# Kernel tuning notes

Measured on AMD Instinct MI355X. Metric: run time of the kernel, lower is better.

The kernel has to match this reference:

```python
import jax, jax.numpy as jnp
import numpy as np

TAU = 0.1
B = 4        # number of batches
S = 256      # spatial extent per axis
K = 128      # max peaks per batch (original caps total at num_batches*128)
NEG = -jnp.inf


def _l2norm(x, eps=1e-12):
    n = jnp.sqrt(jnp.sum(x * x, axis=1, keepdims=True))
    return x / jnp.maximum(n, eps)


def _peak_pool(coords, feats, conf, mask):
    # Submanifold 3x3x3 sparse max-pool on conf and avg-pool on feats,
    # restricted to voxels with conf > tau (the original builds the spconv
    # tensors only from masked voxels). Neighbor lookup via sorted key hash.
    N = coords.shape[0]
    bidx = coords[:, 0]
    x, y, z = coords[:, 1], coords[:, 2], coords[:, 3]
    key = ((bidx * S + x) * S + y) * S + z
    order = jnp.argsort(key)
    skey = key[order]
    hmax = jnp.full((N,), NEG, dtype=conf.dtype)
    fsum = jnp.zeros_like(feats)
    cnt = jnp.zeros((N,), dtype=feats.dtype)
    for dx in (-1, 0, 1):
        for dy in (-1, 0, 1):
            for dz in (-1, 0, 1):
                nx, ny, nz = x + dx, y + dy, z + dz
                valid = (nx >= 0) & (nx < S) & (ny >= 0) & (ny < S) & (nz >= 0) & (nz < S)
                nkey = ((bidx * S + nx) * S + ny) * S + nz
                pos = jnp.minimum(jnp.searchsorted(skey, nkey), N - 1)
                j = order[pos]
                hit = valid & (skey[pos] == nkey) & mask[j]
                hmax = jnp.maximum(hmax, jnp.where(hit, conf[j], NEG))
                fsum = fsum + jnp.where(hit[:, None], feats[j], 0.0)
                cnt = cnt + hit.astype(feats.dtype)
    favg = fsum / jnp.maximum(cnt, 1.0)[:, None]
    return hmax, favg


def setup_inputs() -> dict:
    key = jax.random.key(0)
    ks = jax.random.split(key, 6)
    N, L, D = 800000, 64, 32
    batch = jax.random.randint(ks[0], (N, 1), 0, B, dtype=jnp.int32)
    xyz = jax.random.randint(ks[1], (N, 3), 0, S, dtype=jnp.int32)
    coords = jnp.concatenate([batch, xyz], axis=1)
    voxel_feats = jax.random.normal(ks[2], (N, L), jnp.float32)
    centroid_scores = jax.random.uniform(ks[3], (N, 1), jnp.float32)
    W = jax.random.normal(ks[4], (L, D), jnp.float32) * 0.05
    b = jnp.zeros((D,), jnp.float32)
    background = jax.random.normal(ks[5], (D,), jnp.float32) * 0.02
    return {"coords": coords, "voxel_feats": voxel_feats,
            "centroid_scores": centroid_scores, "W": W, "b": b,
            "background": background}


def reference(coords, voxel_feats, centroid_scores, W, b, background):
    conf = centroid_scores[:, 0]
    mask = conf > TAU
    hmax, peak_feats = _peak_pool(coords, voxel_feats, conf, mask)
    # CenterNet-style NMS: a masked voxel is a peak if it equals its local max
    peak_mask = mask & (hmax == conf)
    voxel_desc = _l2norm(voxel_feats @ W + b)           # [N, D]
    bidx = coords[:, 0]
    peak_conf, blocks = [], []
    for bi in range(B):
        score = jnp.where(peak_mask & (bidx == bi), conf, NEG)
        vals, idx = jax.lax.top_k(score, K)             # fixed K peaks/batch
        valid = jnp.isfinite(vals)
        cdesc = _l2norm(peak_feats[idx] @ W + b)        # [K, D]
        cdesc = jnp.where(valid[:, None], cdesc, 0.0)
        # per-batch layout: background descriptor first, then centroids
        blocks.append(jnp.concatenate([background[None, :], cdesc], axis=0))
        peak_conf.append(jnp.where(valid, vals, 0.0))
    full_desc = jnp.concatenate(blocks, axis=0)         # [B*(K+1), D]
    return jnp.stack(peak_conf, axis=0), voxel_desc, full_desc
```

## Files before the change

kernel.cpp:

```cpp
#include <hip/hip_runtime.h>
#include <math.h>

#define S 256
#define NB 4
#define TAU 0.1f
#define KSEL 128
#define LOG_TAB 21
#define TAB_SZ (1u << LOG_TAB)
#define TAB_MASK (TAB_SZ - 1)
#define EMPTY64 0xFFFFFFFFFFFFFFFFull
#define BM_WORDS (1u << 21)
#define NBINS 8192
#define BIN_BASE 0x3D800
#define CAND_CAP 4096
#define CPAD 32

typedef unsigned long long u64;
typedef unsigned int u32;

__device__ __forceinline__ u32 hash_key(int key) {
    u32 h = (u32)key * 0x9E3779B1u;
    h ^= h >> 15;
    return h & TAB_MASK;
}

__device__ __forceinline__ int conf_bin(float conf) {
    int bin = (int)(__float_as_uint(conf) >> 12) - BIN_BASE;
    return bin < 0 ? 0 : (bin > NBINS - 1 ? NBINS - 1 : bin);
}

__device__ __forceinline__ int tab_lookup(const u64* __restrict__ tab, int key) {
    u32 slot = hash_key(key);
    for (;;) {
        u64 e = tab[slot];
        if ((u32)(e >> 32) == (u32)key) return (int)(u32)e;
        if (e == EMPTY64) return -1;
        slot = (slot + 1) & TAB_MASK;
    }
}

__device__ __forceinline__ void desc_row(const float* __restrict__ feats,
                                         const float* __restrict__ W,
                                         const float* __restrict__ bias,
                                         float* __restrict__ voxel_desc, int i, int N) {
    if (i >= N) return;
    const float4* row4 = (const float4*)(feats + (size_t)i * 64);
    float4 r[16];
    #pragma unroll
    for (int k = 0; k < 16; k++) r[k] = row4[k];
    __builtin_amdgcn_sched_barrier(0);
    float acc[32];
    #pragma unroll
    for (int d = 0; d < 32; d++) acc[d] = bias[d];
    #pragma unroll
    for (int k = 0; k < 16; k++) {
        float4 f = r[k];
        const float* Wb = W + k * 4 * 32;
        #pragma unroll
        for (int d = 0; d < 32; d++) {
            acc[d] = fmaf(f.x, Wb[d], acc[d]);
            acc[d] = fmaf(f.y, Wb[32 + d], acc[d]);
            acc[d] = fmaf(f.z, Wb[64 + d], acc[d]);
            acc[d] = fmaf(f.w, Wb[96 + d], acc[d]);
        }
    }
    float ss = 0.f;
    #pragma unroll
    for (int d = 0; d < 32; d++) ss += acc[d] * acc[d];
    float inv = 1.0f / fmaxf(sqrtf(ss), 1e-12f);
    float4* out4 = (float4*)(voxel_desc + (size_t)i * 32);
    #pragma unroll
    for (int q = 0; q < 8; q++) {
        float4 o;
        o.x = acc[q * 4 + 0] * inv; o.y = acc[q * 4 + 1] * inv;
        o.z = acc[q * 4 + 2] * inv; o.w = acc[q * 4 + 3] * inv;
        out4[q] = o;
    }
}

__device__ __forceinline__ void insert_pt(const int* __restrict__ coords,
                                          const float* __restrict__ scores,
                                          u64* __restrict__ tab, u32* __restrict__ bm,
                                          int i, int N) {
    if (i >= N) return;
    int4 c = ((const int4*)coords)[i];
    float conf = scores[i];
    int key = ((c.x * S + c.y) * S + c.z) * S + c.w;
    if (conf > TAU) atomicOr(&bm[(u32)key >> 5], 1u << (key & 31));
    u64 ins = ((u64)(u32)key << 32) | (u32)i;
    u32 slot = hash_key(key);
    for (;;) {
        u64 e = tab[slot];
        if ((u32)(e >> 32) == (u32)key) { atomicMin(&tab[slot], ins); return; }
        if (e == EMPTY64) {
            u64 prev = atomicCAS(&tab[slot], EMPTY64, ins);
            if (prev == EMPTY64) return;
            if ((u32)(prev >> 32) == (u32)key) { atomicMin(&tab[slot], ins); return; }
        }
        slot = (slot + 1) & TAB_MASK;
    }
}

__global__ __launch_bounds__(256, 4) void k_ins_desc(const int* __restrict__ coords,
        const float* __restrict__ scores, u64* __restrict__ tab, u32* __restrict__ bm,
        const float* __restrict__ feats, const float* __restrict__ W,
        const float* __restrict__ bias, float* __restrict__ voxel_desc,
        int N, int nIns, int nDesc, int descRow0) {
    int g = blockIdx.x / 3, r = blockIdx.x % 3;
    if (r < 2) {
        int ib = g * 2 + r;
        if (ib >= nIns) return;
        insert_pt(coords, scores, tab, bm, ib * 256 + threadIdx.x, N);
    } else {
        if (g >= nDesc) return;
        desc_row(feats, W, bias, voxel_desc, descRow0 + g * 256 + threadIdx.x, N);
    }
}

__device__ __forceinline__ void peak_block(const int* __restrict__ coords,
        const float* __restrict__ scores, const u64* __restrict__ tab,
        const u32* __restrict__ bm, u64* __restrict__ peaks, int* __restrict__ cnt,
        int* __restrict__ hist, int N, int pcap, int pb) {
    int i = pb * 256 + threadIdx.x;
    bool alive = (i < N);
    int ii = alive ? i : 0;
    int4 c = ((const int4*)coords)[ii];
    float conf = alive ? scores[ii] : -1.0f;
    int kb = ((c.x * S + c.y) * S + c.z) * S + c.w;
    bool ispeak = false;
    if (alive && conf > TAU) {
        u32 m27 = 0;
        u32 vzm = (u32)((c.w > 0) ? 1 : 0) | 2u | (u32)((c.w < S - 1) ? 4 : 0);
        #pragma unroll
        for (int dx = -1; dx <= 1; dx++) {
            if ((unsigned)(c.y + dx) >= S) continue;
            #pragma unroll
            for (int dy = -1; dy <= 1; dy++) {
                if ((unsigned)(c.z + dy) >= S) continue;
                int nk = kb + dx * (S * S) + dy * S;
                u32 idx = (u32)nk >> 5;
                int sft = nk & 31;
                u32 w0 = bm[idx];
                u32 b3;
                if (sft >= 1 && sft <= 30) {
                    b3 = (w0 >> (sft - 1)) & 7u;
                } else if (sft == 0) {
                    u32 wm = (nk >= 32) ? bm[idx - 1] : 0u;
                    b3 = ((wm >> 31) & 1u) | ((w0 & 3u) << 1);
                } else {
                    u32 wp = (idx + 1 < BM_WORDS) ? bm[idx + 1] : 0u;
                    b3 = ((w0 >> 30) & 3u) | ((wp & 1u) << 2);
                }
                b3 &= vzm;
                int p = ((dx + 1) * 3 + (dy + 1)) * 3;
                m27 |= b3 << p;
            }
        }
        int j0 = tab_lookup(tab, kb);
        float hmax = (j0 == i) ? conf : scores[j0];
        m27 &= ~(1u << 13);
        while (m27) {
            int q = __builtin_ctz(m27);
            m27 &= m27 - 1;
            int dx = q / 9 - 1;
            int rr = q % 9;
            int dy = rr / 3 - 1, dz = rr % 3 - 1;
            int j = tab_lookup(tab, kb + dx * (S * S) + dy * S + dz);
            if (j >= 0) hmax = fmaxf(hmax, scores[j]);
        }
        ispeak = (hmax == conf);
    }

    if (ispeak) atomicAdd(&hist[c.x * NBINS + conf_bin(conf)], 1);

    __shared__ int wcnt[4][NB];
    __shared__ int bbase[NB];
    int w = threadIdx.x >> 6;
    int lane = threadIdx.x & 63;
    u64 lmask_lt = (lane == 63) ? 0x7FFFFFFFFFFFFFFFull : ((1ull << lane) - 1ull);
    u64 mb[NB];
    #pragma unroll
    for (int b = 0; b < NB; b++) {
        mb[b] = __ballot(ispeak && (c.x == b));
        if (lane == 0) wcnt[w][b] = __popcll(mb[b]);
    }
    __syncthreads();
    if (threadIdx.x < NB) {
        int b = threadIdx.x;
        int tot = wcnt[0][b] + wcnt[1][b] + wcnt[2][b] + wcnt[3][b];
        bbase[b] = tot > 0 ? atomicAdd(&cnt[b * CPAD], tot) : 0;
    }
    __syncthreads();
    if (ispeak) {
        int b = c.x;
        int pre = 0;
        for (int w2 = 0; w2 < w; w2++) pre += wcnt[w2][b];
        int rank = __popcll(mb[b] & lmask_lt);
        int pidx = bbase[b] + pre + rank;
        if (pidx < pcap)
            peaks[(size_t)b * pcap + pidx] =
                ((u64)__float_as_uint(conf) << 32) | (u32)(~(u32)i);
    }
}

__global__ __launch_bounds__(256, 4) void k_peak_desc(const int* __restrict__ coords,
        const float* __restrict__ scores, const u64* __restrict__ tab,
        const u32* __restrict__ bm, u64* __restrict__ peaks, int* __restrict__ cnt,
        int* __restrict__ hist, const float* __restrict__ feats,
        const float* __restrict__ W, const float* __restrict__ bias,
        float* __restrict__ voxel_desc, int N, int pcap,
        int nPeak, int nDesc, int descRow0) {
    int g = blockIdx.x / 3, r = blockIdx.x % 3;
    if (r < 2) {
        int pb = g * 2 + r;
        if (pb >= nPeak) return;
        peak_block(coords, scores, tab, bm, peaks, cnt, hist, N, pcap, pb);
    } else {
        if (g >= nDesc) return;
        desc_row(feats, W, bias, voxel_desc, descRow0 + g * 256 + threadIdx.x, N);
    }
}

__global__ void k_thresh(const int* __restrict__ hist, const int* __restrict__ cnt,
                         u32* __restrict__ thrbin, int pcap) {
    int w = threadIdx.x >> 6;
    int lane = threadIdx.x & 63;
    if (w >= NB) return;
    int n = cnt[w * CPAD]; if (n > pcap) n = pcap;
    int need = n < KSEL ? n : KSEL;
    const int* h = hist + w * NBINS;
    int running = 0;
    u32 thr = 0;
    for (int hi = NBINS - 64; hi >= 0; hi -= 64) {
        int v = h[hi + lane];
        int s = v;
        #pragma unroll
        for (int off = 1; off < 64; off <<= 1) {
            int o = __shfl_down(s, off);
            if (lane + off < 64) s += o;
        }
        int csum = __shfl(s, 0);
        if (running + csum >= need) {
            u64 m = __ballot(running + s >= need);
            int top = 63 - __builtin_clzll(m);
            thr = (u32)(hi + top);
            break;
        }
        running += csum;
    }
    if (lane == 0) thrbin[w] = thr;
}

__global__ void k_compact(const u64* __restrict__ peaks, const int* __restrict__ cnt,
                          const u32* __restrict__ thrbin, u64* __restrict__ cand,
                          int* __restrict__ ccnt, int pcap) {
    int t = blockIdx.x * blockDim.x + threadIdx.x;
    int b = t / pcap;
    if (b >= NB) return;
    int e = t % pcap;
    int n = cnt[b * CPAD]; if (n > pcap) n = pcap;
    if (e >= n) return;
    u64 key = peaks[(size_t)b * pcap + e];
    float conf = __uint_as_float((u32)(key >> 32));
    if (conf_bin(conf) >= (int)thrbin[b]) {
        int p = atomicAdd(&ccnt[b * CPAD], 1);
        if (p < CAND_CAP) cand[(size_t)b * CAND_CAP + p] = key;
    }
}

__global__ void k_topk(u64* __restrict__ cand, const int* __restrict__ ccnt,
                       u64* __restrict__ bufA, u64* __restrict__ selected) {
    int b = blockIdx.x;
    int tid = threadIdx.x;
    __shared__ int hist[256];
    __shared__ int sh_split, sh_above, sh_selc, sh_candc;
    u64* sel = selected + b * KSEL;
    u64* pcur = cand + (size_t)b * CAND_CAP;
    u64* pnxt = bufA + (size_t)b * CAND_CAP;
    int n = ccnt[b * CPAD];
    if (n > CAND_CAP) n = CAND_CAP;
    int need = KSEL, nsel = 0;

    for (int byte = 7; byte >= 0; byte--) {
        if (need <= 0) break;
        if (n <= need) {
            for (int idx = tid; idx < n; idx += blockDim.x) sel[nsel + idx] = pcur[idx];
            nsel += n; need -= n; n = 0;
            break;
        }
        hist[tid] = 0;
        __syncthreads();
        int shift = byte * 8;
        for (int idx = tid; idx < n; idx += blockDim.x)
            atomicAdd(&hist[(int)((pcur[idx] >> shift) & 255)], 1);
        __syncthreads();
        if (tid == 0) {
            int above = 0, s = 255;
            for (; s > 0; s--) {
                if (above + hist[s] >= need) break;
                above += hist[s];
            }
            sh_split = s; sh_above = above; sh_selc = 0; sh_candc = 0;
        }
        __syncthreads();
        int s = sh_split;
        for (int idx = tid; idx < n; idx += blockDim.x) {
            u64 e = pcur[idx];
            int bv = (int)((e >> shift) & 255);
            if (bv > s) { int p = atomicAdd(&sh_selc, 1); sel[nsel + p] = e; }
            else if (bv == s) { int p = atomicAdd(&sh_candc, 1); pnxt[p] = e; }
        }
        __syncthreads();
        nsel += sh_above; need -= sh_above; n = sh_candc;
        u64* t = pcur; pcur = pnxt; pnxt = t;
        __syncthreads();
    }
    if (need > 0 && n > 0) {
        int take = need < n ? need : n;
        for (int idx = tid; idx < take; idx += blockDim.x) sel[nsel + idx] = pcur[idx];
        nsel += take;
    }
    for (int idx = nsel + tid; idx < KSEL; idx += blockDim.x) sel[idx] = 0;
    __syncthreads();

    __shared__ u64 sk[KSEL];
    if (tid < KSEL) sk[tid] = sel[tid];
    __syncthreads();
    for (int k = 2; k <= KSEL; k <<= 1) {
        for (int j = k >> 1; j > 0; j >>= 1) {
            if (tid < KSEL) {
                int ixj = tid ^ j;
                if (ixj > tid) {
                    u64 a = sk[tid], c2 = sk[ixj];
                    bool upper = (tid & k) != 0;
                    if (upper ? (a > c2) : (a < c2)) { sk[tid] = c2; sk[ixj] = a; }
                }
            }
            __syncthreads();
        }
    }
    if (tid < KSEL) sel[tid] = sk[tid];
}

__global__ void k_final(const int* __restrict__ coords, const float* __restrict__ feats,
                        const float* __restrict__ scores, const float* __restrict__ W,
                        const float* __restrict__ bias, const float* __restrict__ background,
                        const u64* __restrict__ tab, const u64* __restrict__ selected,
                        float* __restrict__ out, int N) {
    int gw = (blockIdx.x * blockDim.x + threadIdx.x) >> 6;
    int lane = threadIdx.x & 63;
    float* full = out + NB * KSEL + (size_t)N * 32;
    if (gw >= NB * KSEL) {
        int b = gw - NB * KSEL;
        if (b < NB && lane < 32)
            full[(size_t)(b * (KSEL + 1)) * 32 + lane] = background[lane];
        return;
    }
    int b = gw >> 7, k = gw & 127;
    u64 key = selected[gw];
    float* row = full + (size_t)(b * (KSEL + 1) + 1 + k) * 32;
    if (key == 0ull) {
        if (lane == 0) out[gw] = 0.f;
        if (lane < 32) row[lane] = 0.f;
        return;
    }
    float conf = __uint_as_float((u32)(key >> 32));
    int i = (int)(~(u32)key);
    if (lane == 0) out[gw] = conf;
    int4 c = ((const int4*)coords)[i];
    int kb = ((c.x * S + c.y) * S + c.z) * S + c.w;
    int j = -1; bool hit = false;
    if (lane < 27) {
        int dx = lane / 9 - 1, r = lane % 9;
        int dy = r / 3 - 1, dz = r % 3 - 1;
        int nx = c.y + dx, ny = c.z + dy, nz = c.w + dz;
        if ((unsigned)nx < S && (unsigned)ny < S && (unsigned)nz < S) {
            j = tab_lookup(tab, kb + dx * (S * S) + dy * S + dz);
            if (j >= 0) hit = scores[j] > TAU;
        }
    }
    u64 hm = __ballot(hit);
    int c27 = __popcll(hm);
    float fsum = 0.f;
    u64 m = hm;
    while (m) {
        int src = __ffsll((long long)m) - 1;
        m &= m - 1;
        int jj = __shfl(j, src);
        fsum += feats[(size_t)jj * 64 + lane];
    }
    float favg = fsum / fmaxf((float)c27, 1.0f);
    int d = lane & 31;
    float acc = bias[d];
    #pragma unroll
    for (int l = 0; l < 64; l++) {
        float fl = __shfl(favg, l);
        acc = fmaf(fl, W[l * 32 + d], acc);
    }
    float ss = acc * acc;
    #pragma unroll
    for (int off = 1; off < 32; off <<= 1) ss += __shfl_xor(ss, off);
    float inv = 1.0f / fmaxf(sqrtf(ss), 1e-12f);
    if (lane < 32) row[lane] = acc * inv;
}

extern "C" void kernel_launch(void* const* d_in, const int* in_sizes, int n_in,
                              void* d_out, int out_size, void* d_ws, size_t ws_size,
                              hipStream_t stream) {
    const int* coords = (const int*)d_in[0];
    const float* feats = (const float*)d_in[1];
    const float* scores = (const float*)d_in[2];
    const float* W = (const float*)d_in[3];
    const float* bias = (const float*)d_in[4];
    const float* background = (const float*)d_in[5];
    int N = in_sizes[0] / 4;
    float* out = (float*)d_out;
    int pcap = N / 2;

    char* ws = (char*)d_ws;
    size_t off = 0;
    u64* tab = (u64*)(ws + off); off += (size_t)TAB_SZ * 8;
    size_t zoff = off;
    u32* bm = (u32*)(ws + off); off += (size_t)BM_WORDS * 4;
    int* hist = (int*)(ws + off); off += (size_t)NB * NBINS * 4;
    int* cnt = (int*)(ws + off); off += (size_t)NB * CPAD * 4;
    int* ccnt = (int*)(ws + off); off += (size_t)NB * CPAD * 4;
    u32* thrbin = (u32*)(ws + off); off += 256;
    size_t zlen = off - zoff;
    u64* peaks = (u64*)(ws + off); off += (size_t)NB * pcap * 8;
    u64* cand = (u64*)(ws + off); off += (size_t)NB * CAND_CAP * 8;
    u64* bufA = (u64*)(ws + off); off += (size_t)NB * CAND_CAP * 8;
    u64* selected = (u64*)(ws + off); off += (size_t)NB * KSEL * 8;

    int nBlk = (N + 255) / 256;
    int nDescA = nBlk / 2;
    int rowsA = nDescA * 256;
    int nDescB = (N - rowsA + 255) / 256;
    int half = (nBlk + 1) / 2;
    int g1 = half > nDescA ? half : nDescA;
    int g2 = half > nDescB ? half : nDescB;

    (void)hipMemsetAsync(tab, 0xFF, (size_t)TAB_SZ * 8, stream);
    (void)hipMemsetAsync(ws + zoff, 0, zlen, stream);
    k_ins_desc<<<3 * g1, 256, 0, stream>>>(coords, scores, tab, bm,
                                           feats, W, bias, out + NB * KSEL,
                                           N, nBlk, nDescA, 0);
    k_peak_desc<<<3 * g2, 256, 0, stream>>>(coords, scores, tab, bm, peaks, cnt, hist,
                                            feats, W, bias, out + NB * KSEL,
                                            N, pcap, nBlk, nDescB, rowsA);
    k_thresh<<<1, 256, 0, stream>>>(hist, cnt, thrbin, pcap);
    k_compact<<<(NB * pcap + 255) / 256, 256, 0, stream>>>(peaks, cnt, thrbin, cand, ccnt, pcap);
    k_topk<<<NB, 256, 0, stream>>>(cand, ccnt, bufA, selected);
    k_final<<<(NB * KSEL + NB + 3) / 4, 256, 0, stream>>>(coords, feats, scores, W, bias,
                                                          background, tab, selected, out, N);
}
```

Baseline: 281.3 us.

## Store occupancy bitmap as 8x8x8 bricks for neighborhood lookup

Replaces the linear z-row occupancy bitmap with a brick layout where each 64-bit word holds an 8x8 y-z plane slice of an 8x8x8 brick. The 3x3x3 neighbor occupancy test in the peak kernel now reads one word per touched brick per x-slice, usually 3 words instead of 9 rows with boundary handling, which improves locality. In exchange it adds nested loops with data-dependent branches and bit extraction per neighbor, which may cost more ALU time and cause divergence at brick edges.

```diff
diff --git a/kernel.cpp b/kernel.cpp
--- a/kernel.cpp
+++ b/kernel.cpp
@@ -9,7 +9,7 @@
 #define TAB_SZ (1u << LOG_TAB)
 #define TAB_MASK (TAB_SZ - 1)
 #define EMPTY64 0xFFFFFFFFFFFFFFFFull
-#define BM_WORDS (1u << 21)
+#define BMQ_WORDS (1u << 20)
 #define NBINS 8192
 #define BIN_BASE 0x3D800
 #define CAND_CAP 4096
@@ -80,13 +80,17 @@
 
 __device__ __forceinline__ void insert_pt(const int* __restrict__ coords,
                                           const float* __restrict__ scores,
-                                          u64* __restrict__ tab, u32* __restrict__ bm,
+                                          u64* __restrict__ tab, u64* __restrict__ bmq,
                                           int i, int N) {
     if (i >= N) return;
     int4 c = ((const int4*)coords)[i];
     float conf = scores[i];
     int key = ((c.x * S + c.y) * S + c.z) * S + c.w;
-    if (conf > TAU) atomicOr(&bm[(u32)key >> 5], 1u << (key & 31));
+    if (conf > TAU) {
+        int brick = (((c.x << 5) + (c.y >> 3)) * 32 + (c.z >> 3)) * 32 + (c.w >> 3);
+        u64 bit = 1ull << (((c.z & 7) << 3) | (c.w & 7));
+        atomicOr(&bmq[brick * 8 + (c.y & 7)], bit);
+    }
     u64 ins = ((u64)(u32)key << 32) | (u32)i;
     u32 slot = hash_key(key);
     for (;;) {
@@ -102,7 +106,7 @@
 }
 
 __global__ __launch_bounds__(256, 4) void k_ins_desc(const int* __restrict__ coords,
-        const float* __restrict__ scores, u64* __restrict__ tab, u32* __restrict__ bm,
+        const float* __restrict__ scores, u64* __restrict__ tab, u64* __restrict__ bmq,
         const float* __restrict__ feats, const float* __restrict__ W,
         const float* __restrict__ bias, float* __restrict__ voxel_desc,
         int N, int nIns, int nDesc, int descRow0) {
@@ -110,7 +114,7 @@
     if (r < 2) {
         int ib = g * 2 + r;
         if (ib >= nIns) return;
-        insert_pt(coords, scores, tab, bm, ib * 256 + threadIdx.x, N);
+        insert_pt(coords, scores, tab, bmq, ib * 256 + threadIdx.x, N);
     } else {
         if (g >= nDesc) return;
         desc_row(feats, W, bias, voxel_desc, descRow0 + g * 256 + threadIdx.x, N);
@@ -119,41 +123,45 @@
 
 __device__ __forceinline__ void peak_block(const int* __restrict__ coords,
         const float* __restrict__ scores, const u64* __restrict__ tab,
-        const u32* __restrict__ bm, u64* __restrict__ peaks, int* __restrict__ cnt,
+        const u64* __restrict__ bmq, u64* __restrict__ peaks, int* __restrict__ cnt,
         int* __restrict__ hist, int N, int pcap, int pb) {
     int i = pb * 256 + threadIdx.x;
     bool alive = (i < N);
     int ii = alive ? i : 0;
     int4 c = ((const int4*)coords)[ii];
     float conf = alive ? scores[ii] : -1.0f;
-    int kb = ((c.x * S + c.y) * S + c.z) * S + c.w;
+    int X = c.y, Y = c.z, Z = c.w;
+    int kb = ((c.x * S + X) * S + Y) * S + Z;
     bool ispeak = false;
     if (alive && conf > TAU) {
         u32 m27 = 0;
-        u32 vzm = (u32)((c.w > 0) ? 1 : 0) | 2u | (u32)((c.w < S - 1) ? 4 : 0);
-        #pragma unroll
-        for (int dx = -1; dx <= 1; dx++) {
-            if ((unsigned)(c.y + dx) >= S) continue;
+        int bx0 = (X > 0 ? X - 1 : X) >> 3, bx1 = (X < S - 1 ? X + 1 : X) >> 3;
+        int by0 = (Y > 0 ? Y - 1 : Y) >> 3, by1 = (Y < S - 1 ? Y + 1 : Y) >> 3;
+        int bz0 = (Z > 0 ? Z - 1 : Z) >> 3, bz1 = (Z < S - 1 ? Z + 1 : Z) >> 3;
+        for (int bx = bx0; bx <= bx1; bx++) {
             #pragma unroll
-            for (int dy = -1; dy <= 1; dy++) {
-                if ((unsigned)(c.z + dy) >= S) continue;
-                int nk = kb + dx * (S * S) + dy * S;
-                u32 idx = (u32)nk >> 5;
-                int sft = nk & 31;
-                u32 w0 = bm[idx];
-                u32 b3;
-                if (sft >= 1 && sft <= 30) {
-                    b3 = (w0 >> (sft - 1)) & 7u;
-                } else if (sft == 0) {
-                    u32 wm = (nk >= 32) ? bm[idx - 1] : 0u;
-                    b3 = ((wm >> 31) & 1u) | ((w0 & 3u) << 1);
-                } else {
-                    u32 wp = (idx + 1 < BM_WORDS) ? bm[idx + 1] : 0u;
-                    b3 = ((w0 >> 30) & 3u) | ((wp & 1u) << 2);
+            for (int dx = -1; dx <= 1; dx++) {
+                int nx = X + dx;
+                if ((unsigned)nx >= S || (nx >> 3) != bx) continue;
+                int wsel = nx & 7;
+                for (int by = by0; by <= by1; by++) {
+                    for (int bz = bz0; bz <= bz1; bz++) {
+                        u64 w = bmq[((((c.x << 5) + bx) * 32 + by) * 32 + bz) * 8 + wsel];
+                        if (!w) continue;
+                        #pragma unroll
+                        for (int dy = -1; dy <= 1; dy++) {
+                            int ny = Y + dy;
+                            if ((unsigned)ny >= S || (ny >> 3) != by) continue;
+                            #pragma unroll
+                            for (int dz = -1; dz <= 1; dz++) {
+                                int nz = Z + dz;
+                                if ((unsigned)nz >= S || (nz >> 3) != bz) continue;
+                                if ((w >> (((ny & 7) << 3) | (nz & 7))) & 1ull)
+                                    m27 |= 1u << (((dx + 1) * 3 + (dy + 1)) * 3 + (dz + 1));
+                            }
+                        }
+                    }
                 }
-                b3 &= vzm;
-                int p = ((dx + 1) * 3 + (dy + 1)) * 3;
-                m27 |= b3 << p;
             }
         }
         int j0 = tab_lookup(tab, kb);
@@ -205,7 +213,7 @@
 
 __global__ __launch_bounds__(256, 4) void k_peak_desc(const int* __restrict__ coords,
         const float* __restrict__ scores, const u64* __restrict__ tab,
-        const u32* __restrict__ bm, u64* __restrict__ peaks, int* __restrict__ cnt,
+        const u64* __restrict__ bmq, u64* __restrict__ peaks, int* __restrict__ cnt,
         int* __restrict__ hist, const float* __restrict__ feats,
         const float* __restrict__ W, const float* __restrict__ bias,
         float* __restrict__ voxel_desc, int N, int pcap,
@@ -214,7 +222,7 @@
     if (r < 2) {
         int pb = g * 2 + r;
         if (pb >= nPeak) return;
-        peak_block(coords, scores, tab, bm, peaks, cnt, hist, N, pcap, pb);
+        peak_block(coords, scores, tab, bmq, peaks, cnt, hist, N, pcap, pb);
     } else {
         if (g >= nDesc) return;
         desc_row(feats, W, bias, voxel_desc, descRow0 + g * 256 + threadIdx.x, N);
@@ -421,7 +429,7 @@
     size_t off = 0;
     u64* tab = (u64*)(ws + off); off += (size_t)TAB_SZ * 8;
     size_t zoff = off;
-    u32* bm = (u32*)(ws + off); off += (size_t)BM_WORDS * 4;
+    u64* bmq = (u64*)(ws + off); off += (size_t)BMQ_WORDS * 8;
     int* hist = (int*)(ws + off); off += (size_t)NB * NBINS * 4;
     int* cnt = (int*)(ws + off); off += (size_t)NB * CPAD * 4;
     int* ccnt = (int*)(ws + off); off += (size_t)NB * CPAD * 4;
@@ -442,10 +450,10 @@
 
     (void)hipMemsetAsync(tab, 0xFF, (size_t)TAB_SZ * 8, stream);
     (void)hipMemsetAsync(ws + zoff, 0, zlen, stream);
-    k_ins_desc<<<3 * g1, 256, 0, stream>>>(coords, scores, tab, bm,
+    k_ins_desc<<<3 * g1, 256, 0, stream>>>(coords, scores, tab, bmq,
                                            feats, W, bias, out + NB * KSEL,
                                            N, nBlk, nDescA, 0);
-    k_peak_desc<<<3 * g2, 256, 0, stream>>>(coords, scores, tab, bm, peaks, cnt, hist,
+    k_peak_desc<<<3 * g2, 256, 0, stream>>>(coords, scores, tab, bmq, peaks, cnt, hist,
                                             feats, W, bias, out + NB * KSEL,
                                             N, pcap, nBlk, nDescB, rowsA);
     k_thresh<<<1, 256, 0, stream>>>(hist, cnt, thrbin, pcap);
```

Result: no change. 278.7 us (-0.9%).
